# Optimization experiments

Hardware: AMD Instinct MI355X
Metric: run time of the kernel (lower is better)

## Reference

```python
import jax, jax.numpy as jnp
import numpy as np

N_NODES = 50000


def gcn_conv(x, edge_index, W, b, n_nodes):
    """PyG GCNConv: add self-loops, symmetric deg normalization, gather-scatter."""
    src, dst = edge_index[0], edge_index[1]
    loop = jnp.arange(n_nodes, dtype=src.dtype)
    src = jnp.concatenate([src, loop])
    dst = jnp.concatenate([dst, loop])
    # transform first (in -> hidden), then propagate
    h = x @ W  # [N, H]
    ones = jnp.ones_like(dst, dtype=h.dtype)
    deg = jax.ops.segment_sum(ones, dst, num_segments=n_nodes)  # [N]
    dinv = jnp.where(deg > 0, jax.lax.rsqrt(deg), 0.0)
    norm = dinv[src] * dinv[dst]  # [E+N]
    msg = h[src] * norm[:, None]  # [E+N, H] gather + scale
    out = jax.ops.segment_sum(msg, dst, num_segments=n_nodes)  # scatter-add
    return out + b


def setup_inputs() -> dict:
    key = jax.random.key(0)
    ks = jax.random.split(key, 5)
    N, E, C_in, H, C_out = N_NODES, 800000, 128, 128, 1
    x = jax.random.normal(ks[0], (N, C_in), dtype=jnp.float32)
    edge_index = jax.random.randint(ks[1], (2, E), 0, N, dtype=jnp.int32)
    sc_in = 1.0 / np.sqrt(C_in)
    sc_h = 1.0 / np.sqrt(H)
    W_gcn = jax.random.normal(ks[2], (C_in, H), dtype=jnp.float32) * sc_in
    b_gcn = jnp.zeros((H,), dtype=jnp.float32)
    W1 = jax.random.normal(ks[3], (H, H), dtype=jnp.float32) * sc_h
    b1 = jnp.zeros((H,), dtype=jnp.float32)
    W2 = jax.random.normal(ks[4], (H, C_out), dtype=jnp.float32) * sc_h
    b2 = jnp.zeros((C_out,), dtype=jnp.float32)
    return {"x": x, "edge_index": edge_index, "W_gcn": W_gcn, "b_gcn": b_gcn,
            "W1": W1, "b1": b1, "W2": W2, "b2": b2}


def reference(x, edge_index, W_gcn, b_gcn, W1, b1, W2, b2):
    n_nodes = x.shape[0]
    h = jax.nn.relu(gcn_conv(x, edge_index, W_gcn, b_gcn, n_nodes))
    h = jax.nn.relu(h @ W1 + b1)
    return h @ W2 + b2
```

## Files before the change

kernel.cpp:

```cpp
#include <hip/hip_runtime.h>
#include <hip/hip_bf16.h>

#define HID 128
#define EPB 2048
#define BSH 5
#define NROWS 32
#define CAP 768
#define NBMAX 1600
#define SROW 136

typedef __attribute__((ext_vector_type(8))) short bf16x8;
typedef __attribute__((ext_vector_type(4))) float f32x4;

static inline size_t align256(size_t x) { return (x + 255) & ~(size_t)255; }

__device__ __forceinline__ unsigned short f2bf(float f) {
    unsigned int u = __float_as_uint(f);
    unsigned int r = (u + 0x7fffu + ((u >> 16) & 1u)) >> 16;
    return (unsigned short)r;
}
__device__ __forceinline__ float2 bf2x2(unsigned int u) {
    return make_float2(__uint_as_float(u << 16), __uint_as_float(u & 0xffff0000u));
}

__global__ void k_prep(const float* __restrict__ W, const float* __restrict__ W1,
                       unsigned short* __restrict__ WT, unsigned short* __restrict__ W1T,
                       int* __restrict__ gbase, int nbuck) {
    int idx = blockIdx.x * 256 + threadIdx.x;
    if (idx < HID * HID) {
        int k = idx >> 7, n = idx & 127;
        WT[n * HID + k]  = f2bf(W[idx]);
        W1T[n * HID + k] = f2bf(W1[idx]);
    }
    if (idx < nbuck) gbase[idx] = idx * CAP;
}

__global__ __launch_bounds__(256) void k_gemm_bin(
        const float* __restrict__ x, const unsigned short* __restrict__ WT,
        unsigned short* __restrict__ hs, int N,
        const int* __restrict__ src, const int* __restrict__ dst, int E,
        int* __restrict__ gbase, unsigned int* __restrict__ ebuf,
        int nbuck, int gemm_blocks) {
    __shared__ int sh_h[NBMAX], sh_cur[NBMAX];
    int bid = blockIdx.x;
    if (bid < gemm_blocks) {
        int tid = threadIdx.x;
        int wid = tid >> 6, lane = tid & 63;
        int m = lane & 15, q = lane >> 4;
        int row0 = bid * 64 + wid * 16;
        int arow_i = row0 + m;
        bool rvalid = arow_i < N;
        const float* arow = x + (size_t)arow_i * HID;
        f32x4 acc[8];
#pragma unroll
        for (int t = 0; t < 8; t++) acc[t] = (f32x4){0.f, 0.f, 0.f, 0.f};
#pragma unroll
        for (int c = 0; c < 4; c++) {
            bf16x8 a;
            if (rvalid) {
                float4 f0 = *(const float4*)(arow + c * 32 + q * 8);
                float4 f1 = *(const float4*)(arow + c * 32 + q * 8 + 4);
                a = (bf16x8){(short)f2bf(f0.x), (short)f2bf(f0.y), (short)f2bf(f0.z), (short)f2bf(f0.w),
                             (short)f2bf(f1.x), (short)f2bf(f1.y), (short)f2bf(f1.z), (short)f2bf(f1.w)};
            } else {
                a = (bf16x8){0, 0, 0, 0, 0, 0, 0, 0};
            }
#pragma unroll
            for (int t = 0; t < 8; t++) {
                bf16x8 b = *(const bf16x8*)(WT + (size_t)(t * 16 + m) * HID + c * 32 + q * 8);
                acc[t] = __builtin_amdgcn_mfma_f32_16x16x32_bf16(a, b, acc[t], 0, 0, 0);
            }
        }
#pragma unroll
        for (int t = 0; t < 8; t++) {
#pragma unroll
            for (int r = 0; r < 4; r++) {
                int rr = row0 + q * 4 + r;
                if (rr < N) hs[(size_t)rr * HID + t * 16 + m] = f2bf(acc[t][r]);
            }
        }
        return;
    }
    int blk = bid - gemm_blocks;
    int t = threadIdx.x;
    for (int i = t; i < nbuck; i += 256) sh_h[i] = 0;
    __syncthreads();
    int e0 = blk * EPB;
    bool full = (e0 + EPB <= E);
    int s[8], d[8];
    if (full) {
        int4 sa = ((const int4*)(src + e0))[t * 2];
        int4 sb = ((const int4*)(src + e0))[t * 2 + 1];
        int4 da = ((const int4*)(dst + e0))[t * 2];
        int4 db = ((const int4*)(dst + e0))[t * 2 + 1];
        s[0] = sa.x; s[1] = sa.y; s[2] = sa.z; s[3] = sa.w;
        s[4] = sb.x; s[5] = sb.y; s[6] = sb.z; s[7] = sb.w;
        d[0] = da.x; d[1] = da.y; d[2] = da.z; d[3] = da.w;
        d[4] = db.x; d[5] = db.y; d[6] = db.z; d[7] = db.w;
    } else {
#pragma unroll
        for (int i = 0; i < 8; i++) {
            int e = e0 + t * 8 + i;
            s[i] = (e < E) ? src[e] : 0;
            d[i] = (e < E) ? dst[e] : 0;
        }
    }
#pragma unroll
    for (int i = 0; i < 8; i++) {
        int e = e0 + t * 8 + i;
        if (e < E) atomicAdd(&sh_h[d[i] >> BSH], 1);
    }
    __syncthreads();
    for (int i = t; i < nbuck; i += 256) {
        int v = sh_h[i];
        if (v) sh_cur[i] = atomicAdd(&gbase[i], v);
    }
    __syncthreads();
#pragma unroll
    for (int i = 0; i < 8; i++) {
        int e = e0 + t * 8 + i;
        if (e < E) {
            int b = d[i] >> BSH;
            int p = atomicAdd(&sh_cur[b], 1);
            ebuf[p] = (unsigned int)s[i] | ((unsigned int)d[i] << 16);
        }
    }
}

__global__ __launch_bounds__(256) void k_dinv(const unsigned int* __restrict__ ebuf,
                                              const int* __restrict__ gbase,
                                              float* __restrict__ dinv, int N) {
    __shared__ int cnt[NROWS];
    int k = blockIdx.x, t = threadIdx.x;
    if (t < NROWS) cnt[t] = 0;
    __syncthreads();
    int e0 = k * CAP, e1 = gbase[k];
#pragma unroll
    for (int i = 0; i < 3; i++) {
        int e = e0 + t + i * 256;
        if (e < e1) atomicAdd(&cnt[(ebuf[e] >> 16) & (NROWS - 1)], 1);
    }
    __syncthreads();
    if (t < NROWS) {
        int node = (k << BSH) + t;
        if (node < N) dinv[node] = rsqrtf((float)cnt[t] + 1.0f);
    }
}

__global__ __launch_bounds__(256) void k_prop_mlp(
        const unsigned short* __restrict__ hs,
        const unsigned int* __restrict__ ebuf, const int* __restrict__ gbase,
        const float* __restrict__ dinv,
        const float* __restrict__ b_gcn,
        const unsigned short* __restrict__ W1T,
        const float* __restrict__ b1, const float* __restrict__ W2,
        const float* __restrict__ b2,
        float* __restrict__ out, int N) {
    __shared__ int sE[CAP];
    __shared__ int scnt[NROWS], scur[NROWS], srow0[NROWS];
    __shared__ __align__(16) unsigned short stage[NROWS * SROW];
    __shared__ float sb1[128], sW2[128];
    int k = blockIdx.x, tid = threadIdx.x;
    int node0 = k << BSH;
    int wid = tid >> 6, lane = tid & 63;
    int g = lane >> 4;
    int fl = lane & 15;

    if (tid < NROWS) scnt[tid] = 0;
    if (tid < 128) { sb1[tid] = b1[tid]; sW2[tid] = W2[tid]; }
    __syncthreads();

    int e0 = k * CAP, e1 = gbase[k];
    unsigned int ue[3];
#pragma unroll
    for (int i = 0; i < 3; i++) {
        int e = e0 + tid + i * 256;
        ue[i] = (e < e1) ? ebuf[e] : 0xffffffffu;
    }
#pragma unroll
    for (int i = 0; i < 3; i++)
        if (ue[i] != 0xffffffffu) atomicAdd(&scnt[(ue[i] >> 16) & (NROWS - 1)], 1);
    __syncthreads();
    if (tid < NROWS) {
        int v = scnt[tid];
        int sc = v;
#pragma unroll
        for (int off = 1; off < NROWS; off <<= 1) {
            int u = __shfl_up(sc, off);
            if (tid >= off) sc += u;
        }
        int excl = sc - v;
        scur[tid] = excl;
        srow0[tid] = excl;
    }
    __syncthreads();
#pragma unroll
    for (int i = 0; i < 3; i++) {
        if (ue[i] != 0xffffffffu) {
            int r = (int)((ue[i] >> 16) & (NROWS - 1));
            int pos = atomicAdd(&scur[r], 1);
            sE[pos] = (int)(ue[i] & 0xffffu);
        }
    }
    __syncthreads();

    const uint4* hsv = (const uint4*)hs;
    float4 b0 = *(const float4*)(b_gcn + fl * 8);
    float4 b1v = *(const float4*)(b_gcn + fl * 8 + 4);
    for (int r = wid * 8; r < wid * 8 + 8; r++) {
        int s0 = srow0[r], s1 = scur[r];
        int node = node0 + r;
        bool rv = node < N;
        float di = rv ? dinv[node] : 0.f;
        float a0 = 0.f, a1 = 0.f, a2 = 0.f, a3 = 0.f, a4 = 0.f, a5 = 0.f, a6 = 0.f, a7 = 0.f;
        int j = s0;
        for (; j + 16 <= s1; j += 16) {
            int eA = sE[j + g], eB = sE[j + 4 + g];
            int eC = sE[j + 8 + g], eD = sE[j + 12 + g];
            float dA = dinv[eA], dB = dinv[eB], dC = dinv[eC], dD = dinv[eD];
            uint4 uA = hsv[(size_t)eA * 16 + fl];
            uint4 uB = hsv[(size_t)eB * 16 + fl];
            uint4 uC = hsv[(size_t)eC * 16 + fl];
            uint4 uD = hsv[(size_t)eD * 16 + fl];
            float2 f;
            f = bf2x2(uA.x); a0 += dA * f.x; a1 += dA * f.y;
            f = bf2x2(uA.y); a2 += dA * f.x; a3 += dA * f.y;
            f = bf2x2(uA.z); a4 += dA * f.x; a5 += dA * f.y;
            f = bf2x2(uA.w); a6 += dA * f.x; a7 += dA * f.y;
            f = bf2x2(uB.x); a0 += dB * f.x; a1 += dB * f.y;
            f = bf2x2(uB.y); a2 += dB * f.x; a3 += dB * f.y;
            f = bf2x2(uB.z); a4 += dB * f.x; a5 += dB * f.y;
            f = bf2x2(uB.w); a6 += dB * f.x; a7 += dB * f.y;
            f = bf2x2(uC.x); a0 += dC * f.x; a1 += dC * f.y;
            f = bf2x2(uC.y); a2 += dC * f.x; a3 += dC * f.y;
            f = bf2x2(uC.z); a4 += dC * f.x; a5 += dC * f.y;
            f = bf2x2(uC.w); a6 += dC * f.x; a7 += dC * f.y;
            f = bf2x2(uD.x); a0 += dD * f.x; a1 += dD * f.y;
            f = bf2x2(uD.y); a2 += dD * f.x; a3 += dD * f.y;
            f = bf2x2(uD.z); a4 += dD * f.x; a5 += dD * f.y;
            f = bf2x2(uD.w); a6 += dD * f.x; a7 += dD * f.y;
        }
        for (; j + 8 <= s1; j += 8) {
            int eA = sE[j + g], eB = sE[j + 4 + g];
            float dA = dinv[eA], dB = dinv[eB];
            uint4 uA = hsv[(size_t)eA * 16 + fl];
            uint4 uB = hsv[(size_t)eB * 16 + fl];
            float2 f;
            f = bf2x2(uA.x); a0 += dA * f.x; a1 += dA * f.y;
            f = bf2x2(uA.y); a2 += dA * f.x; a3 += dA * f.y;
            f = bf2x2(uA.z); a4 += dA * f.x; a5 += dA * f.y;
            f = bf2x2(uA.w); a6 += dA * f.x; a7 += dA * f.y;
            f = bf2x2(uB.x); a0 += dB * f.x; a1 += dB * f.y;
            f = bf2x2(uB.y); a2 += dB * f.x; a3 += dB * f.y;
            f = bf2x2(uB.z); a4 += dB * f.x; a5 += dB * f.y;
            f = bf2x2(uB.w); a6 += dB * f.x; a7 += dB * f.y;
        }
        for (; j + g < s1; j += 4) {
            int ei = sE[j + g];
            float dA = dinv[ei];
            uint4 u = hsv[(size_t)ei * 16 + fl];
            float2 f;
            f = bf2x2(u.x); a0 += dA * f.x; a1 += dA * f.y;
            f = bf2x2(u.y); a2 += dA * f.x; a3 += dA * f.y;
            f = bf2x2(u.z); a4 += dA * f.x; a5 += dA * f.y;
            f = bf2x2(u.w); a6 += dA * f.x; a7 += dA * f.y;
        }
        if (g == 0 && rv) {
            uint4 u = hsv[(size_t)node * 16 + fl];
            float2 f;
            f = bf2x2(u.x); a0 += di * f.x; a1 += di * f.y;
            f = bf2x2(u.y); a2 += di * f.x; a3 += di * f.y;
            f = bf2x2(u.z); a4 += di * f.x; a5 += di * f.y;
            f = bf2x2(u.w); a6 += di * f.x; a7 += di * f.y;
        }
#pragma unroll
        for (int off = 16; off <= 32; off <<= 1) {
            a0 += __shfl_xor(a0, off); a1 += __shfl_xor(a1, off);
            a2 += __shfl_xor(a2, off); a3 += __shfl_xor(a3, off);
            a4 += __shfl_xor(a4, off); a5 += __shfl_xor(a5, off);
            a6 += __shfl_xor(a6, off); a7 += __shfl_xor(a7, off);
        }
        if (g == 0) {
            uint4 o;
            o.x = (unsigned int)f2bf(fmaxf(di * a0 + b0.x, 0.f)) | ((unsigned int)f2bf(fmaxf(di * a1 + b0.y, 0.f)) << 16);
            o.y = (unsigned int)f2bf(fmaxf(di * a2 + b0.z, 0.f)) | ((unsigned int)f2bf(fmaxf(di * a3 + b0.w, 0.f)) << 16);
            o.z = (unsigned int)f2bf(fmaxf(di * a4 + b1v.x, 0.f)) | ((unsigned int)f2bf(fmaxf(di * a5 + b1v.y, 0.f)) << 16);
            o.w = (unsigned int)f2bf(fmaxf(di * a6 + b1v.z, 0.f)) | ((unsigned int)f2bf(fmaxf(di * a7 + b1v.w, 0.f)) << 16);
            *(uint4*)(stage + r * SROW + fl * 8) = o;
        }
    }
    __syncthreads();

    if (wid < 2) {
        int m = lane & 15, q = lane >> 4;
        int row = wid * 16 + m;
        f32x4 acc[8];
#pragma unroll
        for (int t = 0; t < 8; t++) acc[t] = (f32x4){0.f, 0.f, 0.f, 0.f};
#pragma unroll
        for (int c = 0; c < 4; c++) {
            bf16x8 a = *(const bf16x8*)(stage + row * SROW + c * 32 + q * 8);
#pragma unroll
            for (int t = 0; t < 8; t++) {
                bf16x8 b = *(const bf16x8*)(W1T + (size_t)(t * 16 + m) * HID + c * 32 + q * 8);
                acc[t] = __builtin_amdgcn_mfma_f32_16x16x32_bf16(a, b, acc[t], 0, 0, 0);
            }
        }
        float part[4] = {0.f, 0.f, 0.f, 0.f};
#pragma unroll
        for (int t = 0; t < 8; t++) {
            int nc = t * 16 + m;
            float w2 = sW2[nc], bb = sb1[nc];
#pragma unroll
            for (int r2 = 0; r2 < 4; r2++)
                part[r2] += fmaxf(acc[t][r2] + bb, 0.f) * w2;
        }
#pragma unroll
        for (int off = 8; off >= 1; off >>= 1) {
#pragma unroll
            for (int r2 = 0; r2 < 4; r2++) part[r2] += __shfl_xor(part[r2], off);
        }
        if (m == 0) {
            float bb = b2[0];
#pragma unroll
            for (int r2 = 0; r2 < 4; r2++) {
                int rr = node0 + wid * 16 + q * 4 + r2;
                if (rr < N) out[rr] = part[r2] + bb;
            }
        }
    }
}

extern "C" void kernel_launch(void* const* d_in, const int* in_sizes, int n_in,
                              void* d_out, int out_size, void* d_ws, size_t ws_size,
                              hipStream_t stream) {
    const float* x     = (const float*)d_in[0];
    const int*   ei    = (const int*)d_in[1];
    const float* W_gcn = (const float*)d_in[2];
    const float* b_gcn = (const float*)d_in[3];
    const float* W1    = (const float*)d_in[4];
    const float* b1    = (const float*)d_in[5];
    const float* W2    = (const float*)d_in[6];
    const float* b2    = (const float*)d_in[7];
    float* out = (float*)d_out;

    int N = in_sizes[0] / HID;
    int E = in_sizes[1] / 2;
    const int* e_src = ei;
    const int* e_dst = ei + E;
    int NBUCK = (N + NROWS - 1) >> BSH;
    int NBLK = (E + EPB - 1) / EPB;

    char* ws = (char*)d_ws;
    size_t off = 0;
    unsigned short* hs = (unsigned short*)(ws + off);      off = align256(off + (size_t)N * HID * 2);
    float* dinv = (float*)(ws + off);                      off = align256(off + (size_t)N * 4);
    int* gbase = (int*)(ws + off);                         off = align256(off + (size_t)NBUCK * 4);
    unsigned int* ebuf = (unsigned int*)(ws + off);        off = align256(off + (size_t)NBUCK * CAP * 4);
    unsigned short* WT = (unsigned short*)(ws + off);      off = align256(off + (size_t)HID * HID * 2);
    unsigned short* W1T = (unsigned short*)(ws + off);     off = align256(off + (size_t)HID * HID * 2);

    int mfma_blocks = (N + 63) / 64;

    k_prep<<<(HID * HID + 255) / 256, 256, 0, stream>>>(W_gcn, W1, WT, W1T, gbase, NBUCK);

    k_gemm_bin<<<mfma_blocks + NBLK, 256, 0, stream>>>(x, WT, hs, N, e_src, e_dst, E,
                                                       gbase, ebuf, NBUCK, mfma_blocks);

    k_dinv<<<NBUCK, 256, 0, stream>>>(ebuf, gbase, dinv, N);

    k_prop_mlp<<<NBUCK, 256, 0, stream>>>(hs, ebuf, gbase, dinv, b_gcn, W1T, b1, W2, b2, out, N);
}
```

Baseline: 167.0 us.

## Bin edges into coarse 512-node chunks and prewarm the hidden-feature cache

```diff
diff --git a/kernel.cpp b/kernel.cpp
--- a/kernel.cpp
+++ b/kernel.cpp
@@ -5,8 +5,11 @@
 #define EPB 2048
 #define BSH 5
 #define NROWS 32
-#define CAP 768
-#define NBMAX 1600
+#define CAPF 768
+#define CSH 9
+#define FPC 16
+#define CAP_C 8960
+#define NC_MAX 128
 #define SROW 136
 
 typedef __attribute__((ext_vector_type(8))) short bf16x8;
@@ -25,14 +28,14 @@
 
 __global__ void k_prep(const float* __restrict__ W, const float* __restrict__ W1,
                        unsigned short* __restrict__ WT, unsigned short* __restrict__ W1T,
-                       int* __restrict__ gbase, int nbuck) {
+                       int* __restrict__ gbase, int nc) {
     int idx = blockIdx.x * 256 + threadIdx.x;
     if (idx < HID * HID) {
         int k = idx >> 7, n = idx & 127;
         WT[n * HID + k]  = f2bf(W[idx]);
         W1T[n * HID + k] = f2bf(W1[idx]);
     }
-    if (idx < nbuck) gbase[idx] = idx * CAP;
+    if (idx < nc) gbase[idx] = idx * CAP_C;
 }
 
 __global__ __launch_bounds__(256) void k_gemm_bin(
@@ -40,8 +43,8 @@
         unsigned short* __restrict__ hs, int N,
         const int* __restrict__ src, const int* __restrict__ dst, int E,
         int* __restrict__ gbase, unsigned int* __restrict__ ebuf,
-        int nbuck, int gemm_blocks) {
-    __shared__ int sh_h[NBMAX], sh_cur[NBMAX];
+        int nc, int gemm_blocks) {
+    __shared__ int sh_h[NC_MAX], sh_cur[NC_MAX];
     int bid = blockIdx.x;
     if (bid < gemm_blocks) {
         int tid = threadIdx.x;
@@ -83,7 +86,7 @@
     }
     int blk = bid - gemm_blocks;
     int t = threadIdx.x;
-    for (int i = t; i < nbuck; i += 256) sh_h[i] = 0;
+    if (t < nc) sh_h[t] = 0;
     __syncthreads();
     int e0 = blk * EPB;
     bool full = (e0 + EPB <= E);
@@ -108,43 +111,55 @@
 #pragma unroll
     for (int i = 0; i < 8; i++) {
         int e = e0 + t * 8 + i;
-        if (e < E) atomicAdd(&sh_h[d[i] >> BSH], 1);
-    }
-    __syncthreads();
-    for (int i = t; i < nbuck; i += 256) {
-        int v = sh_h[i];
-        if (v) sh_cur[i] = atomicAdd(&gbase[i], v);
+        if (e < E) atomicAdd(&sh_h[d[i] >> CSH], 1);
+    }
+    __syncthreads();
+    if (t < nc) {
+        int v = sh_h[t];
+        if (v) sh_cur[t] = atomicAdd(&gbase[t], v);
     }
     __syncthreads();
 #pragma unroll
     for (int i = 0; i < 8; i++) {
         int e = e0 + t * 8 + i;
         if (e < E) {
-            int b = d[i] >> BSH;
+            int b = d[i] >> CSH;
             int p = atomicAdd(&sh_cur[b], 1);
             ebuf[p] = (unsigned int)s[i] | ((unsigned int)d[i] << 16);
         }
     }
 }
 
-__global__ __launch_bounds__(256) void k_dinv(const unsigned int* __restrict__ ebuf,
-                                              const int* __restrict__ gbase,
-                                              float* __restrict__ dinv, int N) {
-    __shared__ int cnt[NROWS];
-    int k = blockIdx.x, t = threadIdx.x;
-    if (t < NROWS) cnt[t] = 0;
-    __syncthreads();
-    int e0 = k * CAP, e1 = gbase[k];
-#pragma unroll
-    for (int i = 0; i < 3; i++) {
-        int e = e0 + t + i * 256;
-        if (e < e1) atomicAdd(&cnt[(ebuf[e] >> 16) & (NROWS - 1)], 1);
-    }
-    __syncthreads();
-    if (t < NROWS) {
-        int node = (k << BSH) + t;
-        if (node < N) dinv[node] = rsqrtf((float)cnt[t] + 1.0f);
-    }
+__global__ __launch_bounds__(256) void k_dinv_warm(const unsigned int* __restrict__ ebuf,
+                                                   const int* __restrict__ gbase,
+                                                   float* __restrict__ dinv,
+                                                   const unsigned int* __restrict__ hsw,
+                                                   int hs_dwords, int N, int nc) {
+    int b = blockIdx.x, t = threadIdx.x;
+    if (b < nc) {
+        __shared__ int cnt[1 << CSH];
+        cnt[t] = 0; cnt[t + 256] = 0;
+        __syncthreads();
+        int e0 = b * CAP_C, e1 = gbase[b];
+        for (int e = e0 + t; e < e1; e += 256)
+            atomicAdd(&cnt[(ebuf[e] >> 16) & ((1 << CSH) - 1)], 1);
+        __syncthreads();
+#pragma unroll
+        for (int i = 0; i < 2; i++) {
+            int node = (b << CSH) + t + i * 256;
+            if (node < N) dinv[node] = rsqrtf((float)cnt[t + i * 256] + 1.0f);
+        }
+        return;
+    }
+    int nsweep = gridDim.x - nc;
+    const uint4* hv = (const uint4*)hsw;
+    int nvec = hs_dwords >> 2;
+    unsigned acc = 0;
+    for (int i = (b - nc) * 256 + t; i < nvec; i += nsweep * 256) {
+        uint4 u = hv[i];
+        acc ^= u.x ^ u.y ^ u.z ^ u.w;
+    }
+    asm volatile("" :: "v"(acc));
 }
 
 __global__ __launch_bounds__(256) void k_prop_mlp(
@@ -156,7 +171,7 @@
         const float* __restrict__ b1, const float* __restrict__ W2,
         const float* __restrict__ b2,
         float* __restrict__ out, int N) {
-    __shared__ int sE[CAP];
+    __shared__ int sE[CAPF];
     __shared__ int scnt[NROWS], scur[NROWS], srow0[NROWS];
     __shared__ __align__(16) unsigned short stage[NROWS * SROW];
     __shared__ float sb1[128], sW2[128];
@@ -170,16 +185,13 @@
     if (tid < 128) { sb1[tid] = b1[tid]; sW2[tid] = W2[tid]; }
     __syncthreads();
 
-    int e0 = k * CAP, e1 = gbase[k];
-    unsigned int ue[3];
-#pragma unroll
-    for (int i = 0; i < 3; i++) {
-        int e = e0 + tid + i * 256;
-        ue[i] = (e < e1) ? ebuf[e] : 0xffffffffu;
-    }
-#pragma unroll
-    for (int i = 0; i < 3; i++)
-        if (ue[i] != 0xffffffffu) atomicAdd(&scnt[(ue[i] >> 16) & (NROWS - 1)], 1);
+    int c = k >> (CSH - BSH);
+    int e0c = c * CAP_C, e1c = gbase[c];
+    for (int e = e0c + tid; e < e1c; e += 256) {
+        unsigned int w = ebuf[e];
+        if ((w >> (16 + BSH)) == (unsigned int)k)
+            atomicAdd(&scnt[(w >> 16) & (NROWS - 1)], 1);
+    }
     __syncthreads();
     if (tid < NROWS) {
         int v = scnt[tid];
@@ -194,12 +206,11 @@
         srow0[tid] = excl;
     }
     __syncthreads();
-#pragma unroll
-    for (int i = 0; i < 3; i++) {
-        if (ue[i] != 0xffffffffu) {
-            int r = (int)((ue[i] >> 16) & (NROWS - 1));
-            int pos = atomicAdd(&scur[r], 1);
-            sE[pos] = (int)(ue[i] & 0xffffu);
+    for (int e = e0c + tid; e < e1c; e += 256) {
+        unsigned int w = ebuf[e];
+        if ((w >> (16 + BSH)) == (unsigned int)k) {
+            int r = (int)((w >> 16) & (NROWS - 1));
+            sE[atomicAdd(&scur[r], 1)] = (int)(w & 0xffffu);
         }
     }
     __syncthreads();
@@ -298,19 +309,19 @@
 #pragma unroll
         for (int t = 0; t < 8; t++) acc[t] = (f32x4){0.f, 0.f, 0.f, 0.f};
 #pragma unroll
-        for (int c = 0; c < 4; c++) {
-            bf16x8 a = *(const bf16x8*)(stage + row * SROW + c * 32 + q * 8);
+        for (int cc = 0; cc < 4; cc++) {
+            bf16x8 a = *(const bf16x8*)(stage + row * SROW + cc * 32 + q * 8);
 #pragma unroll
             for (int t = 0; t < 8; t++) {
-                bf16x8 b = *(const bf16x8*)(W1T + (size_t)(t * 16 + m) * HID + c * 32 + q * 8);
+                bf16x8 b = *(const bf16x8*)(W1T + (size_t)(t * 16 + m) * HID + cc * 32 + q * 8);
                 acc[t] = __builtin_amdgcn_mfma_f32_16x16x32_bf16(a, b, acc[t], 0, 0, 0);
             }
         }
         float part[4] = {0.f, 0.f, 0.f, 0.f};
 #pragma unroll
         for (int t = 0; t < 8; t++) {
-            int nc = t * 16 + m;
-            float w2 = sW2[nc], bb = sb1[nc];
+            int nc2 = t * 16 + m;
+            float w2 = sW2[nc2], bb = sb1[nc2];
 #pragma unroll
             for (int r2 = 0; r2 < 4; r2++)
                 part[r2] += fmaxf(acc[t][r2] + bb, 0.f) * w2;
@@ -348,26 +359,28 @@
     int E = in_sizes[1] / 2;
     const int* e_src = ei;
     const int* e_dst = ei + E;
-    int NBUCK = (N + NROWS - 1) >> BSH;
+    int NBUCK_F = (N + NROWS - 1) >> BSH;
+    int NC = (N + (1 << CSH) - 1) >> CSH;
     int NBLK = (E + EPB - 1) / EPB;
 
     char* ws = (char*)d_ws;
     size_t off = 0;
     unsigned short* hs = (unsigned short*)(ws + off);      off = align256(off + (size_t)N * HID * 2);
     float* dinv = (float*)(ws + off);                      off = align256(off + (size_t)N * 4);
-    int* gbase = (int*)(ws + off);                         off = align256(off + (size_t)NBUCK * 4);
-    unsigned int* ebuf = (unsigned int*)(ws + off);        off = align256(off + (size_t)NBUCK * CAP * 4);
+    int* gbase = (int*)(ws + off);                         off = align256(off + (size_t)NC * 4);
+    unsigned int* ebuf = (unsigned int*)(ws + off);        off = align256(off + (size_t)NC * CAP_C * 4);
     unsigned short* WT = (unsigned short*)(ws + off);      off = align256(off + (size_t)HID * HID * 2);
     unsigned short* W1T = (unsigned short*)(ws + off);     off = align256(off + (size_t)HID * HID * 2);
 
     int mfma_blocks = (N + 63) / 64;
 
-    k_prep<<<(HID * HID + 255) / 256, 256, 0, stream>>>(W_gcn, W1, WT, W1T, gbase, NBUCK);
+    k_prep<<<(HID * HID + 255) / 256, 256, 0, stream>>>(W_gcn, W1, WT, W1T, gbase, NC);
 
     k_gemm_bin<<<mfma_blocks + NBLK, 256, 0, stream>>>(x, WT, hs, N, e_src, e_dst, E,
-                                                       gbase, ebuf, NBUCK, mfma_blocks);
-
-    k_dinv<<<NBUCK, 256, 0, stream>>>(ebuf, gbase, dinv, N);
-
-    k_prop_mlp<<<NBUCK, 256, 0, stream>>>(hs, ebuf, gbase, dinv, b_gcn, W1T, b1, W2, b2, out, N);
-}
+                                                       gbase, ebuf, NC, mfma_blocks);
+
+    k_dinv_warm<<<1024, 256, 0, stream>>>(ebuf, gbase, dinv, (const unsigned int*)hs,
+                                          N * HID / 2, N, NC);
+
+    k_prop_mlp<<<NBUCK_F, 256, 0, stream>>>(hs, ebuf, gbase, dinv, b_gcn, W1T, b1, W2, b2, out, N);
+}
```

Result: slower. 201.2 us (+20.4%).
